# Performance work log

Hardware: AMD Instinct MI355X
Metric: run time of the kernel (lower is better)

The kernel has to match this reference:

```python
import jax, jax.numpy as jnp
import numpy as np

N = 100_000      # n_nodes
DEG = 32         # edge_threshold (fixed out-degree)
D = 64           # in_channels = out_channels, heads = 1
NEG_SLOPE = 0.2


def setup_inputs() -> dict:
    key = jax.random.key(0)
    k1, k2, k3, k4 = jax.random.split(key, 4)
    x = jax.random.normal(k1, (N, D), jnp.float32)
    # fixed-degree edge list with no self loops (offset in [1, N-1])
    src = jnp.repeat(jnp.arange(N, dtype=jnp.int64), DEG)
    off = jax.random.randint(k2, (N * DEG,), 1, N, dtype=jnp.int64)
    dst = (src + off) % N
    edge_index = jnp.stack([src, dst])  # [2, E]
    # glorot init as in the torch module
    stdv_w = float(np.sqrt(6.0 / (D + D)))
    weight = jax.random.uniform(k3, (D, D), jnp.float32, -stdv_w, stdv_w)
    stdv_a = float(np.sqrt(6.0 / (1 + 2 * D)))  # att is [1, heads=1, 2*D]
    att = jax.random.uniform(k4, (2 * D,), jnp.float32, -stdv_a, stdv_a)
    bias = jnp.zeros((D,), jnp.float32)
    return {"x": x, "edge_index": edge_index, "weight": weight, "att": att, "bias": bias}


def reference(x, edge_index, weight, att, bias):
    n, d = x.shape
    h = x @ weight                               # [N, D] (heads=1)
    # add self loops (inputs are constructed without self loops)
    loop = jnp.arange(n, dtype=edge_index.dtype)
    src = jnp.concatenate([edge_index[0], loop])  # message sources (x_j)
    dst = jnp.concatenate([edge_index[1], loop])  # aggregation targets (x_i)
    # GAT edge score: (cat([x_i, x_j]) * att).sum(-1) = h_i@a_i + h_j@a_j
    a_i, a_j = att[:d], att[d:]
    s_i = h @ a_i                                 # [N]
    s_j = h @ a_j                                 # [N]
    alpha = s_i[dst] + s_j[src]                   # [E+N]
    alpha = jnp.where(alpha > 0, alpha, NEG_SLOPE * alpha)  # leaky_relu
    # segment softmax over destination nodes (numerically stable)
    amax = jax.ops.segment_max(alpha, dst, num_segments=n)
    e = jnp.exp(alpha - amax[dst])
    denom = jax.ops.segment_sum(e, dst, num_segments=n)
    w = e / (denom[dst] + 1e-16)                  # [E+N]
    # weighted scatter-add aggregation of source features
    out = jax.ops.segment_sum(h[src] * w[:, None], dst, num_segments=n)  # [N, D]
    out = out + bias                              # head-mean is identity (heads=1)
    # dropout(p=0.5) is identity in eval mode; F.normalize (L2, dim=1, eps=1e-12)
    norm = jnp.linalg.norm(out, axis=1, keepdims=True)
    return out / jnp.maximum(norm, 1e-12)
```

## Files before the change

kernel.cpp:

```cpp
#include <hip/hip_runtime.h>
#include <math.h>

#define NEG_SLOPE 0.2f
#define PCHUNK 8192
#define NBINS_MAX 392
#define BIN_CAP 8704

__device__ __forceinline__ unsigned pk_bf16x2(float a, float b) {
    unsigned ua = __float_as_uint(a);
    ua = (ua + 0x7FFFu + ((ua >> 16) & 1u)) >> 16;
    unsigned ub = __float_as_uint(b);
    ub = (ub + 0x7FFFu + ((ub >> 16) & 1u)) & 0xFFFF0000u;
    return ua | ub;
}

__global__ __launch_bounds__(256) void k_linear(const float* __restrict__ x,
        const float* __restrict__ W, const float* __restrict__ att,
        uint2* __restrict__ h16, float* __restrict__ si, float* __restrict__ sj,
        int n)
{
    int tid = threadIdx.x;
    int lane = tid & 63;
    int wv = tid >> 6;
    int q = lane >> 4;
    int f = lane & 15;

    const float4* W4 = (const float4*)W;
    float4 Wr[16];
#pragma unroll
    for (int kb = 0; kb < 16; ++kb)
        Wr[kb] = W4[(16 * q + kb) * 16 + f];

    const float4* att4 = (const float4*)att;
    float4 ai4 = att4[f];
    float4 aj4 = att4[16 + f];
    const float4* x4 = (const float4*)x;

    int row0 = (blockIdx.x * 4 + wv) * 8;
    for (int r = 0; r < 8; ++r) {
        int row = row0 + r;
        if (row >= n) break;
        size_t xb = (size_t)row * 16 + 4 * q;
        float4 xq0 = x4[xb + 0];
        float4 xq1 = x4[xb + 1];
        float4 xq2 = x4[xb + 2];
        float4 xq3 = x4[xb + 3];
        float4 acc = {0.f, 0.f, 0.f, 0.f};
#define LSTEP(xc, kb) { float4 w4 = Wr[kb]; \
        acc.x = fmaf((xc), w4.x, acc.x); acc.y = fmaf((xc), w4.y, acc.y); \
        acc.z = fmaf((xc), w4.z, acc.z); acc.w = fmaf((xc), w4.w, acc.w); }
        LSTEP(xq0.x, 0)  LSTEP(xq0.y, 1)  LSTEP(xq0.z, 2)  LSTEP(xq0.w, 3)
        LSTEP(xq1.x, 4)  LSTEP(xq1.y, 5)  LSTEP(xq1.z, 6)  LSTEP(xq1.w, 7)
        LSTEP(xq2.x, 8)  LSTEP(xq2.y, 9)  LSTEP(xq2.z, 10) LSTEP(xq2.w, 11)
        LSTEP(xq3.x, 12) LSTEP(xq3.y, 13) LSTEP(xq3.z, 14) LSTEP(xq3.w, 15)
#undef LSTEP
        acc.x += __shfl_xor(acc.x, 16); acc.x += __shfl_xor(acc.x, 32);
        acc.y += __shfl_xor(acc.y, 16); acc.y += __shfl_xor(acc.y, 32);
        acc.z += __shfl_xor(acc.z, 16); acc.z += __shfl_xor(acc.z, 32);
        acc.w += __shfl_xor(acc.w, 16); acc.w += __shfl_xor(acc.w, 32);

        if (q == 0) {
            uint2 p;
            p.x = pk_bf16x2(acc.x, acc.y);
            p.y = pk_bf16x2(acc.z, acc.w);
            h16[(size_t)row * 16 + f] = p;
        }

        float p = acc.x * ai4.x + acc.y * ai4.y + acc.z * ai4.z + acc.w * ai4.w;
        float pq = acc.x * aj4.x + acc.y * aj4.y + acc.z * aj4.z + acc.w * aj4.w;
#pragma unroll
        for (int o = 8; o >= 1; o >>= 1) {
            p += __shfl_xor(p, o);
            pq += __shfl_xor(pq, o);
        }
        if (lane == 0) { si[row] = p; sj[row] = pq; }
    }
}

__global__ __launch_bounds__(256) void k_sortbin(const int* __restrict__ src,
        const int* __restrict__ dst, int E, int nbins,
        int* __restrict__ bin_cursor, unsigned* __restrict__ bin_edges)
{
    __shared__ unsigned stage[PCHUNK];
    __shared__ unsigned short sbin[PCHUNK];
    __shared__ int hist[NBINS_MAX];
    __shared__ int off[NBINS_MAX + 1];
    __shared__ int curL[NBINS_MAX];
    __shared__ int gbase[NBINS_MAX];
    __shared__ int wsum[4];

    int tid = threadIdx.x;
    int base = blockIdx.x * PCHUNK;
    int cnt = E - base;
    if (cnt > PCHUNK) cnt = PCHUNK;

    for (int b = tid; b < nbins; b += 256) hist[b] = 0;
    __syncthreads();
    for (int i = tid; i < cnt; i += 256)
        atomicAdd(&hist[dst[base + i] >> 8], 1);
    __syncthreads();

    int lane = tid & 63;
    int wv = tid >> 6;
    int t2 = tid * 2;
    int a = (t2 < nbins) ? hist[t2] : 0;
    int b2 = (t2 + 1 < nbins) ? hist[t2 + 1] : 0;
    int s = a + b2;
    int v = s;
#pragma unroll
    for (int o = 1; o < 64; o <<= 1) {
        int t = __shfl_up(v, o);
        if (lane >= o) v += t;
    }
    if (lane == 63) wsum[wv] = v;
    __syncthreads();
    int woff = 0;
    for (int w = 0; w < wv; ++w) woff += wsum[w];
    int ex = v - s + woff;
    if (t2 <= nbins) off[t2] = ex;
    if (t2 + 1 <= nbins) off[t2 + 1] = ex + a;
    __syncthreads();

    for (int b = tid; b < nbins; b += 256) {
        int c = hist[b];
        int g = (c > 0) ? atomicAdd(&bin_cursor[b], c) : 0;
        gbase[b] = b * BIN_CAP + g;
        curL[b] = off[b];
    }
    __syncthreads();

    for (int i = tid; i < cnt; i += 256) {
        int e = base + i;
        int d = dst[e];
        int bb = d >> 8;
        int pos = atomicAdd(&curL[bb], 1);
        stage[pos] = ((unsigned)(d & 255) << 17) | (unsigned)src[e];
        sbin[pos] = (unsigned short)bb;
    }
    __syncthreads();
    for (int i = tid; i < cnt; i += 256) {
        int bb = sbin[i];
        int w = gbase[bb] + (i - off[bb]);
        if (w < (bb + 1) * BIN_CAP)
            bin_edges[w] = stage[i];
    }
}

__global__ __launch_bounds__(256) void k_csr(const int* __restrict__ bin_cursor,
        unsigned* __restrict__ bin_edges,
        int* __restrict__ row_start, int* __restrict__ deg, int n)
{
    __shared__ unsigned stage[BIN_CAP];
    __shared__ int cnt256[256];
    __shared__ int wsum[4];
    int b = blockIdx.x;
    int tid = threadIdx.x;
    int base = b * BIN_CAP;
    int cntE = bin_cursor[b];
    if (cntE > BIN_CAP) cntE = BIN_CAP;

    for (int i = tid; i < cntE; i += 256) stage[i] = bin_edges[base + i];
    cnt256[tid] = 0;
    __syncthreads();
    for (int i = tid; i < cntE; i += 256)
        atomicAdd(&cnt256[stage[i] >> 17], 1);
    __syncthreads();

    int lane = tid & 63;
    int wv = tid >> 6;
    int s = cnt256[tid];
    int v = s;
#pragma unroll
    for (int o = 1; o < 64; o <<= 1) {
        int t = __shfl_up(v, o);
        if (lane >= o) v += t;
    }
    if (lane == 63) wsum[wv] = v;
    __syncthreads();
    int woff = 0;
    for (int w = 0; w < wv; ++w) woff += wsum[w];
    int ex = v - s + woff;

    int gd = b * 256 + tid;
    if (gd < n) {
        row_start[gd] = base + ex;
        deg[gd] = s;
    }
    __syncthreads();
    cnt256[tid] = ex;
    __syncthreads();
    for (int i = tid; i < cntE; i += 256) {
        unsigned pk = stage[i];
        int pos = atomicAdd(&cnt256[pk >> 17], 1);
        bin_edges[base + pos] = pk & 0x1FFFFu;
    }
}

__global__ __launch_bounds__(256) void k_agg(const uint2* __restrict__ h16,
        const float* __restrict__ si, const float* __restrict__ sj,
        const int* __restrict__ row_start, const int* __restrict__ deg_arr,
        const unsigned* __restrict__ cols,
        const float* __restrict__ bias, float* __restrict__ out, int n)
{
    __shared__ int2 swArr[4][132];
    int lane = threadIdx.x & 63;
    int wv = threadIdx.x >> 6;
    int d = blockIdx.x * 4 + wv;
    if (d >= n) return;

    int dg = deg_arr[d];
    if (dg > 128) dg = 128;
    int rs = row_start[d];
    float sid = si[d];

    int s0 = 0, s1 = 0;
    float a0 = -1e30f, a1 = -1e30f;
    if (lane < dg) {
        s0 = (int)cols[rs + lane];
        float t = sid + sj[s0];
        a0 = t > 0.f ? t : NEG_SLOPE * t;
    }
    if (lane + 64 < dg) {
        s1 = (int)cols[rs + lane + 64];
        float t = sid + sj[s1];
        a1 = t > 0.f ? t : NEG_SLOPE * t;
    }
    float tself = sid + sj[d];
    float aself = tself > 0.f ? tself : NEG_SLOPE * tself;

    float m = fmaxf(fmaxf(a0, a1), aself);
#pragma unroll
    for (int o = 32; o >= 1; o >>= 1) m = fmaxf(m, __shfl_xor(m, o));

    float e0 = (lane < dg) ? __expf(a0 - m) : 0.f;
    float e1 = (lane + 64 < dg) ? __expf(a1 - m) : 0.f;
    float eself = __expf(aself - m);

    float dsum = e0 + e1;
#pragma unroll
    for (int o = 32; o >= 1; o >>= 1) dsum += __shfl_xor(dsum, o);
    dsum += eself;

    if (lane < dg) swArr[wv][lane] = make_int2(s0, __float_as_int(e0));
    if (lane + 64 < dg) swArr[wv][lane + 64] = make_int2(s1, __float_as_int(e1));
    if (lane == 0) swArr[wv][dg] = make_int2(d, __float_as_int(eself));
    int cntAll = dg + 1;

    int q = lane >> 4;
    int f = lane & 15;
    float4 acc0 = {0.f, 0.f, 0.f, 0.f};
    float4 acc1 = {0.f, 0.f, 0.f, 0.f};
    float4 acc2 = {0.f, 0.f, 0.f, 0.f};
    float4 acc3 = {0.f, 0.f, 0.f, 0.f};

#define UNPK_FMA(hv, wgt, acc) { \
        acc.x = fmaf((wgt), __uint_as_float((hv).x << 16), acc.x); \
        acc.y = fmaf((wgt), __uint_as_float((hv).x & 0xFFFF0000u), acc.y); \
        acc.z = fmaf((wgt), __uint_as_float((hv).y << 16), acc.z); \
        acc.w = fmaf((wgt), __uint_as_float((hv).y & 0xFFFF0000u), acc.w); }

    int j = q;
    for (; j + 12 < cntAll; j += 16) {
        int2 eA = swArr[wv][j];
        int2 eB = swArr[wv][j + 4];
        int2 eC = swArr[wv][j + 8];
        int2 eD = swArr[wv][j + 12];
        uint2 hA = h16[(size_t)eA.x * 16 + f];
        uint2 hB = h16[(size_t)eB.x * 16 + f];
        uint2 hC = h16[(size_t)eC.x * 16 + f];
        uint2 hD = h16[(size_t)eD.x * 16 + f];
        float wA = __int_as_float(eA.y);
        float wB = __int_as_float(eB.y);
        float wC = __int_as_float(eC.y);
        float wD = __int_as_float(eD.y);
        UNPK_FMA(hA, wA, acc0)
        UNPK_FMA(hB, wB, acc1)
        UNPK_FMA(hC, wC, acc2)
        UNPK_FMA(hD, wD, acc3)
    }
    for (; j + 4 < cntAll; j += 8) {
        int2 eA = swArr[wv][j];
        int2 eB = swArr[wv][j + 4];
        uint2 hA = h16[(size_t)eA.x * 16 + f];
        uint2 hB = h16[(size_t)eB.x * 16 + f];
        float wA = __int_as_float(eA.y);
        float wB = __int_as_float(eB.y);
        UNPK_FMA(hA, wA, acc0)
        UNPK_FMA(hB, wB, acc1)
    }
    if (j < cntAll) {
        int2 eA = swArr[wv][j];
        uint2 hA = h16[(size_t)eA.x * 16 + f];
        float wA = __int_as_float(eA.y);
        UNPK_FMA(hA, wA, acc0)
    }
#undef UNPK_FMA

    acc0.x += acc1.x; acc0.y += acc1.y; acc0.z += acc1.z; acc0.w += acc1.w;
    acc2.x += acc3.x; acc2.y += acc3.y; acc2.z += acc3.z; acc2.w += acc3.w;
    acc0.x += acc2.x; acc0.y += acc2.y; acc0.z += acc2.z; acc0.w += acc2.w;

    acc0.x += __shfl_xor(acc0.x, 16); acc0.x += __shfl_xor(acc0.x, 32);
    acc0.y += __shfl_xor(acc0.y, 16); acc0.y += __shfl_xor(acc0.y, 32);
    acc0.z += __shfl_xor(acc0.z, 16); acc0.z += __shfl_xor(acc0.z, 32);
    acc0.w += __shfl_xor(acc0.w, 16); acc0.w += __shfl_xor(acc0.w, 32);

    float inv = 1.f / (dsum + 1e-16f);
    const float4* b4 = (const float4*)bias;
    float4 bb = b4[f];
    float4 o4;
    o4.x = acc0.x * inv + bb.x;
    o4.y = acc0.y * inv + bb.y;
    o4.z = acc0.z * inv + bb.z;
    o4.w = acc0.w * inv + bb.w;

    float nsq = o4.x * o4.x + o4.y * o4.y + o4.z * o4.z + o4.w * o4.w;
#pragma unroll
    for (int o = 8; o >= 1; o >>= 1) nsq += __shfl_xor(nsq, o);
    float rn = 1.f / fmaxf(sqrtf(nsq), 1e-12f);

    if (q == 0) {
        float4 res;
        res.x = o4.x * rn; res.y = o4.y * rn; res.z = o4.z * rn; res.w = o4.w * rn;
        ((float4*)out)[(size_t)d * 16 + f] = res;
    }
}

extern "C" void kernel_launch(void* const* d_in, const int* in_sizes, int n_in,
                              void* d_out, int out_size, void* d_ws, size_t ws_size,
                              hipStream_t stream)
{
    const float* x    = (const float*)d_in[0];
    const int*   ei   = (const int*)d_in[1];
    const float* W    = (const float*)d_in[2];
    const float* att  = (const float*)d_in[3];
    const float* bias = (const float*)d_in[4];
    float* out = (float*)d_out;

    int n = in_sizes[0] / 64;
    int E = in_sizes[1] / 2;
    const int* src = ei;
    const int* dst = ei + E;

    int nbins = (n + 255) >> 8;
    int NB = (E + PCHUNK - 1) / PCHUNK;

    char* ws = (char*)d_ws;
#define CARVE(ptr, type, count) type* ptr = (type*)ws; \
        ws += (((size_t)(count) * sizeof(type)) + 255) & ~(size_t)255;
    CARVE(h16, uint2, (size_t)n * 16)
    CARVE(si, float, n)
    CARVE(sj, float, n)
    CARVE(row_start, int, n)
    CARVE(deg, int, n)
    CARVE(bin_cursor, int, NBINS_MAX)
    CARVE(bin_edges, unsigned, (size_t)nbins * BIN_CAP)
#undef CARVE

    hipMemsetAsync(bin_cursor, 0, (size_t)nbins * sizeof(int), stream);
    k_linear<<<(n + 31) / 32, 256, 0, stream>>>(x, W, att, h16, si, sj, n);
    k_sortbin<<<NB, 256, 0, stream>>>(src, dst, E, nbins, bin_cursor, bin_edges);
    k_csr<<<nbins, 256, 0, stream>>>(bin_cursor, bin_edges, row_start, deg, n);
    k_agg<<<(n + 3) / 4, 256, 0, stream>>>(h16, si, sj, row_start, deg, bin_edges, bias, out, n);
}
```

Baseline: 274.5 us.

## Vectorize edge-binning loads, widen sort blocks, fold cursor reset into linear kernel

The bin-cursor memset is dropped and its zeroing moved into k_linear, which removes one stream operation. k_sortbin and k_csr now run 512-thread blocks and read dst/src and bin_edges as int4/uint4 with scalar tails, cutting load instruction count in the histogram, placement and staging passes. The k_agg gather computes h16 addresses with 32-bit shift/or instead of size_t multiplies, trimming address arithmetic. The vector loads assume 16-byte alignment of the index and bin arrays, and larger blocks may lower occupancy given the heavy LDS use.

```diff
diff --git a/kernel.cpp b/kernel.cpp
--- a/kernel.cpp
+++ b/kernel.cpp
@@ -17,9 +17,12 @@
 __global__ __launch_bounds__(256) void k_linear(const float* __restrict__ x,
         const float* __restrict__ W, const float* __restrict__ att,
         uint2* __restrict__ h16, float* __restrict__ si, float* __restrict__ sj,
-        int n)
+        int* __restrict__ bin_cursor, int nbins, int n)
 {
     int tid = threadIdx.x;
+    int g = blockIdx.x * 256 + tid;
+    if (g < nbins) bin_cursor[g] = 0;
+
     int lane = tid & 63;
     int wv = tid >> 6;
     int q = lane >> 4;
@@ -77,7 +80,7 @@
     }
 }
 
-__global__ __launch_bounds__(256) void k_sortbin(const int* __restrict__ src,
+__global__ __launch_bounds__(512) void k_sortbin(const int* __restrict__ src,
         const int* __restrict__ dst, int E, int nbins,
         int* __restrict__ bin_cursor, unsigned* __restrict__ bin_edges)
 {
@@ -87,17 +90,28 @@
     __shared__ int off[NBINS_MAX + 1];
     __shared__ int curL[NBINS_MAX];
     __shared__ int gbase[NBINS_MAX];
-    __shared__ int wsum[4];
+    __shared__ int wsum[8];
 
     int tid = threadIdx.x;
     int base = blockIdx.x * PCHUNK;
     int cnt = E - base;
     if (cnt > PCHUNK) cnt = PCHUNK;
-
-    for (int b = tid; b < nbins; b += 256) hist[b] = 0;
-    __syncthreads();
-    for (int i = tid; i < cnt; i += 256)
-        atomicAdd(&hist[dst[base + i] >> 8], 1);
+    int cnt4 = cnt >> 2;
+
+    for (int b = tid; b < nbins; b += 512) hist[b] = 0;
+    __syncthreads();
+    {
+        const int4* dst4 = (const int4*)(dst + base);
+        for (int i = tid; i < cnt4; i += 512) {
+            int4 d4 = dst4[i];
+            atomicAdd(&hist[d4.x >> 8], 1);
+            atomicAdd(&hist[d4.y >> 8], 1);
+            atomicAdd(&hist[d4.z >> 8], 1);
+            atomicAdd(&hist[d4.w >> 8], 1);
+        }
+        for (int i = (cnt4 << 2) + tid; i < cnt; i += 512)
+            atomicAdd(&hist[dst[base + i] >> 8], 1);
+    }
     __syncthreads();
 
     int lane = tid & 63;
@@ -121,7 +135,7 @@
     if (t2 + 1 <= nbins) off[t2 + 1] = ex + a;
     __syncthreads();
 
-    for (int b = tid; b < nbins; b += 256) {
+    for (int b = tid; b < nbins; b += 512) {
         int c = hist[b];
         int g = (c > 0) ? atomicAdd(&bin_cursor[b], c) : 0;
         gbase[b] = b * BIN_CAP + g;
@@ -129,16 +143,25 @@
     }
     __syncthreads();
 
-    for (int i = tid; i < cnt; i += 256) {
-        int e = base + i;
-        int d = dst[e];
-        int bb = d >> 8;
-        int pos = atomicAdd(&curL[bb], 1);
-        stage[pos] = ((unsigned)(d & 255) << 17) | (unsigned)src[e];
-        sbin[pos] = (unsigned short)bb;
-    }
-    __syncthreads();
-    for (int i = tid; i < cnt; i += 256) {
+    {
+        const int4* dst4 = (const int4*)(dst + base);
+        const int4* src4 = (const int4*)(src + base);
+        for (int i = tid; i < cnt4; i += 512) {
+            int4 d4 = dst4[i];
+            int4 s4 = src4[i];
+#define PLACE(dd, ss) { int bb = (dd) >> 8; int pos = atomicAdd(&curL[bb], 1); \
+            stage[pos] = ((unsigned)((dd) & 255) << 17) | (unsigned)(ss); \
+            sbin[pos] = (unsigned short)bb; }
+            PLACE(d4.x, s4.x) PLACE(d4.y, s4.y) PLACE(d4.z, s4.z) PLACE(d4.w, s4.w)
+        }
+        for (int i = (cnt4 << 2) + tid; i < cnt; i += 512) {
+            int dd = dst[base + i]; int ss = src[base + i];
+            PLACE(dd, ss)
+        }
+#undef PLACE
+    }
+    __syncthreads();
+    for (int i = tid; i < cnt; i += 512) {
         int bb = sbin[i];
         int w = gbase[bb] + (i - off[bb]);
         if (w < (bb + 1) * BIN_CAP)
@@ -146,7 +169,7 @@
     }
 }
 
-__global__ __launch_bounds__(256) void k_csr(const int* __restrict__ bin_cursor,
+__global__ __launch_bounds__(512) void k_csr(const int* __restrict__ bin_cursor,
         unsigned* __restrict__ bin_edges,
         int* __restrict__ row_start, int* __restrict__ deg, int n)
 {
@@ -158,38 +181,47 @@
     int base = b * BIN_CAP;
     int cntE = bin_cursor[b];
     if (cntE > BIN_CAP) cntE = BIN_CAP;
-
-    for (int i = tid; i < cntE; i += 256) stage[i] = bin_edges[base + i];
-    cnt256[tid] = 0;
-    __syncthreads();
-    for (int i = tid; i < cntE; i += 256)
+    int cnt4 = cntE >> 2;
+
+    {
+        const uint4* be4 = (const uint4*)(bin_edges + base);
+        uint4* st4 = (uint4*)stage;
+        for (int i = tid; i < cnt4; i += 512) st4[i] = be4[i];
+        for (int i = (cnt4 << 2) + tid; i < cntE; i += 512) stage[i] = bin_edges[base + i];
+    }
+    if (tid < 256) cnt256[tid] = 0;
+    __syncthreads();
+    for (int i = tid; i < cntE; i += 512)
         atomicAdd(&cnt256[stage[i] >> 17], 1);
     __syncthreads();
 
     int lane = tid & 63;
     int wv = tid >> 6;
-    int s = cnt256[tid];
-    int v = s;
-#pragma unroll
-    for (int o = 1; o < 64; o <<= 1) {
-        int t = __shfl_up(v, o);
-        if (lane >= o) v += t;
-    }
-    if (lane == 63) wsum[wv] = v;
-    __syncthreads();
-    int woff = 0;
-    for (int w = 0; w < wv; ++w) woff += wsum[w];
-    int ex = v - s + woff;
-
-    int gd = b * 256 + tid;
-    if (gd < n) {
-        row_start[gd] = base + ex;
-        deg[gd] = s;
-    }
-    __syncthreads();
-    cnt256[tid] = ex;
-    __syncthreads();
-    for (int i = tid; i < cntE; i += 256) {
+    int s = 0, v = 0;
+    if (tid < 256) {
+        s = cnt256[tid];
+        v = s;
+#pragma unroll
+        for (int o = 1; o < 64; o <<= 1) {
+            int t = __shfl_up(v, o);
+            if (lane >= o) v += t;
+        }
+        if (lane == 63) wsum[wv] = v;
+    }
+    __syncthreads();
+    if (tid < 256) {
+        int woff = 0;
+        for (int w = 0; w < wv; ++w) woff += wsum[w];
+        int ex = v - s + woff;
+        int gd = b * 256 + tid;
+        if (gd < n) {
+            row_start[gd] = base + ex;
+            deg[gd] = s;
+        }
+        cnt256[tid] = ex;
+    }
+    __syncthreads();
+    for (int i = tid; i < cntE; i += 512) {
         unsigned pk = stage[i];
         int pos = atomicAdd(&cnt256[pk >> 17], 1);
         bin_edges[base + pos] = pk & 0x1FFFFu;
@@ -248,11 +280,14 @@
 
     int q = lane >> 4;
     int f = lane & 15;
+    int fb = f << 3;
+    const char* h8 = (const char*)h16;
     float4 acc0 = {0.f, 0.f, 0.f, 0.f};
     float4 acc1 = {0.f, 0.f, 0.f, 0.f};
     float4 acc2 = {0.f, 0.f, 0.f, 0.f};
     float4 acc3 = {0.f, 0.f, 0.f, 0.f};
 
+#define GLOAD(e) (*(const uint2*)(h8 + (((unsigned)(e) << 7) | fb)))
 #define UNPK_FMA(hv, wgt, acc) { \
         acc.x = fmaf((wgt), __uint_as_float((hv).x << 16), acc.x); \
         acc.y = fmaf((wgt), __uint_as_float((hv).x & 0xFFFF0000u), acc.y); \
@@ -265,10 +300,10 @@
         int2 eB = swArr[wv][j + 4];
         int2 eC = swArr[wv][j + 8];
         int2 eD = swArr[wv][j + 12];
-        uint2 hA = h16[(size_t)eA.x * 16 + f];
-        uint2 hB = h16[(size_t)eB.x * 16 + f];
-        uint2 hC = h16[(size_t)eC.x * 16 + f];
-        uint2 hD = h16[(size_t)eD.x * 16 + f];
+        uint2 hA = GLOAD(eA.x);
+        uint2 hB = GLOAD(eB.x);
+        uint2 hC = GLOAD(eC.x);
+        uint2 hD = GLOAD(eD.x);
         float wA = __int_as_float(eA.y);
         float wB = __int_as_float(eB.y);
         float wC = __int_as_float(eC.y);
@@ -281,8 +316,8 @@
     for (; j + 4 < cntAll; j += 8) {
         int2 eA = swArr[wv][j];
         int2 eB = swArr[wv][j + 4];
-        uint2 hA = h16[(size_t)eA.x * 16 + f];
-        uint2 hB = h16[(size_t)eB.x * 16 + f];
+        uint2 hA = GLOAD(eA.x);
+        uint2 hB = GLOAD(eB.x);
         float wA = __int_as_float(eA.y);
         float wB = __int_as_float(eB.y);
         UNPK_FMA(hA, wA, acc0)
@@ -290,11 +325,12 @@
     }
     if (j < cntAll) {
         int2 eA = swArr[wv][j];
-        uint2 hA = h16[(size_t)eA.x * 16 + f];
+        uint2 hA = GLOAD(eA.x);
         float wA = __int_as_float(eA.y);
         UNPK_FMA(hA, wA, acc0)
     }
 #undef UNPK_FMA
+#undef GLOAD
 
     acc0.x += acc1.x; acc0.y += acc1.y; acc0.z += acc1.z; acc0.w += acc1.w;
     acc2.x += acc3.x; acc2.y += acc3.y; acc2.z += acc3.z; acc2.w += acc3.w;
@@ -357,9 +393,8 @@
     CARVE(bin_edges, unsigned, (size_t)nbins * BIN_CAP)
 #undef CARVE
 
-    hipMemsetAsync(bin_cursor, 0, (size_t)nbins * sizeof(int), stream);
-    k_linear<<<(n + 31) / 32, 256, 0, stream>>>(x, W, att, h16, si, sj, n);
-    k_sortbin<<<NB, 256, 0, stream>>>(src, dst, E, nbins, bin_cursor, bin_edges);
-    k_csr<<<nbins, 256, 0, stream>>>(bin_cursor, bin_edges, row_start, deg, n);
+    k_linear<<<(n + 31) / 32, 256, 0, stream>>>(x, W, att, h16, si, sj, bin_cursor, nbins, n);
+    k_sortbin<<<NB, 512, 0, stream>>>(src, dst, E, nbins, bin_cursor, bin_edges);
+    k_csr<<<nbins, 512, 0, stream>>>(bin_cursor, bin_edges, row_start, deg, n);
     k_agg<<<(n + 3) / 4, 256, 0, stream>>>(h16, si, sj, row_start, deg, bin_edges, bias, out, n);
 }
```

Result: faster. 246.0 us (-10.4%).
